# Kernel tuning notes

Measured on AMD Instinct MI355X. Metric: run time of the kernel, lower is better.

The kernel has to match this reference:

```python
import jax, jax.numpy as jnp
import numpy as np

N = 50000      # nodes
E = 800000     # edges (avg degree 16)
D = 64         # num_node_features
H = 64         # hidden_channels
G = 512        # graphs in batch
OUT = 32       # final linear output
NEG_SLOPE = 0.2


def setup_inputs() -> dict:
    key = jax.random.key(0)
    ks = jax.random.split(key, 20)
    s = 0.1  # param init scale
    inp = {
        "x": jax.random.normal(ks[0], (N, D), jnp.float32),
        "edge_index": jax.random.randint(ks[1], (2, E), 0, N, dtype=jnp.int64),
        "batch": jnp.sort(jax.random.randint(ks[2], (N,), 0, G, dtype=jnp.int64)),
        # GATv2 layer 1 (D -> H)
        "Wl1": jax.random.normal(ks[3], (D, H), jnp.float32) * s,
        "bl1": jnp.zeros((H,), jnp.float32),
        "Wr1": jax.random.normal(ks[4], (D, H), jnp.float32) * s,
        "br1": jnp.zeros((H,), jnp.float32),
        "att1": jax.random.normal(ks[5], (H,), jnp.float32) * s,
        "bias1": jnp.zeros((H,), jnp.float32),
        # GATv2 layer 2 (H -> H)
        "Wl2": jax.random.normal(ks[6], (H, H), jnp.float32) * s,
        "bl2": jnp.zeros((H,), jnp.float32),
        "Wr2": jax.random.normal(ks[7], (H, H), jnp.float32) * s,
        "br2": jnp.zeros((H,), jnp.float32),
        "att2": jax.random.normal(ks[8], (H,), jnp.float32) * s,
        "bias2": jnp.zeros((H,), jnp.float32),
        # final classifier
        "lin_w": jax.random.normal(ks[9], (H, OUT), jnp.float32) * s,
        "lin_b": jnp.zeros((OUT,), jnp.float32),
    }
    return inp


def _gatv2(x, src, dst, Wl, bl, Wr, br, att, bias):
    # GATv2Conv, heads=1, PyG semantics: messages flow src -> dst
    xl = x @ Wl + bl                       # [N, H] source transform (also the message)
    xr = x @ Wr + br                       # [N, H] destination transform
    z = xl[src] + xr[dst]                  # [E, H] gather
    e = jax.nn.leaky_relu(z, NEG_SLOPE) @ att  # [E] edge scores
    # segment softmax over edges grouped by destination node
    m = jax.ops.segment_max(e, dst, num_segments=N)   # [N]
    ex = jnp.exp(e - m[dst])                          # [E]
    denom = jax.ops.segment_sum(ex, dst, num_segments=N)  # [N]
    alpha = ex / denom[dst]                            # [E]
    out = jax.ops.segment_sum(alpha[:, None] * xl[src], dst, num_segments=N)  # [N, H]
    return out + bias


def reference(x, edge_index, batch,
              Wl1, bl1, Wr1, br1, att1, bias1,
              Wl2, bl2, Wr2, br2, att2, bias2,
              lin_w, lin_b):
    src, dst = edge_index[0], edge_index[1]
    h = jax.nn.relu(_gatv2(x, src, dst, Wl1, bl1, Wr1, br1, att1, bias1))
    h = jax.nn.relu(_gatv2(h, src, dst, Wl2, bl2, Wr2, br2, att2, bias2))
    # global mean pool over graphs
    sums = jax.ops.segment_sum(h, batch, num_segments=G)          # [G, H]
    cnts = jax.ops.segment_sum(jnp.ones((h.shape[0],), h.dtype), batch, num_segments=G)
    pooled = sums / jnp.maximum(cnts, 1.0)[:, None]
    # dropout(p=0.5) is identity at inference
    return pooled @ lin_w + lin_b                                  # [G, 32]
```

## Files before the change

kernel.cpp:

```cpp
#include <hip/hip_runtime.h>
#include <hip/hip_fp16.h>
#include <math.h>


#define ELLC    48
#define OVF_CAP 65536
#define ECHUNK  2048

typedef int      vint4 __attribute__((ext_vector_type(4)));
typedef _Float16 half4 __attribute__((ext_vector_type(4)));
typedef float    f32x4 __attribute__((ext_vector_type(4)));

#define GROWS 32

__device__ __forceinline__ void stage_rows_f32(
    int row0, int t, const float* __restrict__ X, int n, float* xS) {
    for (int i = t; i < GROWS * 16; i += 256) {
        int r = row0 + (i >> 4);
        f32x4 v;
        v[0] = 0.f; v[1] = 0.f; v[2] = 0.f; v[3] = 0.f;
        if (r < n)
            v = __builtin_nontemporal_load(
                &((const f32x4*)(X + (size_t)r * 64))[i & 15]);
        ((f32x4*)xS)[i] = v;
    }
}

__device__ __forceinline__ void gemm_compute(
    int row0, int t,
    const float* __restrict__ Wl, const float* __restrict__ bl,
    const float* __restrict__ Wr, const float* __restrict__ br,
    _Float16* __restrict__ xl, float* __restrict__ xr, int n,
    const float* xS) {
    int h  = t & 63;
    int rb = t >> 6;
    float accl[8], accr[8];
#pragma unroll
    for (int i = 0; i < 8; ++i) { accl[i] = 0.f; accr[i] = 0.f; }
#pragma unroll 4
    for (int d = 0; d < 64; ++d) {
        float wl = Wl[d * 64 + h];
        float wr = Wr[d * 64 + h];
#pragma unroll
        for (int i = 0; i < 8; ++i) {
            float xv = xS[(rb + 4 * i) * 64 + d];
            accl[i] += xv * wl;
            accr[i] += xv * wr;
        }
    }
    float blv = bl[h], brv = br[h];
#pragma unroll
    for (int i = 0; i < 8; ++i) {
        int r = row0 + rb + 4 * i;
        if (r < n) {
            __builtin_nontemporal_store((_Float16)(accl[i] + blv),
                                        &xl[(size_t)r * 64 + h]);
            __builtin_nontemporal_store(accr[i] + brv,
                                        &xr[(size_t)r * 64 + h]);
        }
    }
}

__global__ __launch_bounds__(256) void fill_gemm_kernel(
    const int* __restrict__ src, const int* __restrict__ dst,
    int* __restrict__ cnt, unsigned short* __restrict__ ell,
    int* __restrict__ novf, int* __restrict__ ovf_dst, int* __restrict__ ovf_src,
    int E, int N, int psize, int fb, int ggrid,
    const float* __restrict__ X,
    const float* __restrict__ Wl, const float* __restrict__ bl,
    const float* __restrict__ Wr, const float* __restrict__ br,
    _Float16* __restrict__ xl, float* __restrict__ xr) {
    __shared__ float xS[GROWS * 64];
    int b = blockIdx.x;
    int q = b / 24, r = b % 24;
    if (r >= 16) {
        int vg = q * 8 + (r - 16);
        if (vg < ggrid) {
            stage_rows_f32(vg * GROWS, threadIdx.x, X, N, xS);
            __syncthreads();
            gemm_compute(vg * GROWS, threadIdx.x, Wl, bl, Wr, br, xl, xr, N, xS);
        }
        return;
    }
    int vb = q * 16 + r;
    if (vb >= fb) return;
    int t     = threadIdx.x;
    int chunk = vb >> 3;
    int p     = vb & 7;
    int d0    = p * psize;
    int d1    = min(N, d0 + psize);
    int e0    = chunk * ECHUNK;
    int e1    = min(E, e0 + ECHUNK);
    int nq    = (e1 - e0) >> 2;
    const vint4* dst4 = (const vint4*)(dst + e0);
    const vint4* src4 = (const vint4*)(src + e0);

    auto scatter4 = [&](vint4 dv, vint4 sv) {
#pragma unroll
        for (int k = 0; k < 4; ++k) {
            int d = dv[k];
            int s = sv[k];
            if (d >= d0 && d < d1) {
                int pos = atomicAdd(&cnt[d], 1);
                if (pos < ELLC) {
                    ell[d * ELLC + pos] = (unsigned short)s;
                } else {
                    int j = atomicAdd(novf, 1);
                    if (j < OVF_CAP) { ovf_dst[j] = d; ovf_src[j] = s; }
                }
            }
        }
    };

    if (nq == (ECHUNK >> 2)) {
        vint4 dvA = __builtin_nontemporal_load(&dst4[t]);
        vint4 svA = __builtin_nontemporal_load(&src4[t]);
        vint4 dvB = __builtin_nontemporal_load(&dst4[t + 256]);
        vint4 svB = __builtin_nontemporal_load(&src4[t + 256]);
        scatter4(dvA, svA);
        scatter4(dvB, svB);
    } else {
        for (int qq = t; qq < nq; qq += 256) {
            vint4 dv = __builtin_nontemporal_load(&dst4[qq]);
            vint4 sv = __builtin_nontemporal_load(&src4[qq]);
            scatter4(dv, sv);
        }
        for (int e = e0 + (nq << 2) + t; e < e1; e += 256) {
            int d = dst[e];
            if (d >= d0 && d < d1) {
                int pos = atomicAdd(&cnt[d], 1);
                int s   = src[e];
                if (pos < ELLC) {
                    ell[d * ELLC + pos] = (unsigned short)s;
                } else {
                    int j = atomicAdd(novf, 1);
                    if (j < OVF_CAP) { ovf_dst[j] = d; ovf_src[j] = s; }
                }
            }
        }
    }
}

__device__ __forceinline__ void agg_row(
    int d, int lane, int g, int l,
    const _Float16* __restrict__ xl, const float* __restrict__ xr,
    const int* __restrict__ cnt, const unsigned short* __restrict__ ell,
    const int* __restrict__ novf, const int* __restrict__ ovf_dst,
    const int* __restrict__ ovf_src,
    float4 att4, float& s, float4& acc, int& deg_d) {
    deg_d = cnt[d];
    int nd  = min(deg_d, ELLC);
    int beg = d * ELLC;
    s = 0.f;
    acc = make_float4(0.f, 0.f, 0.f, 0.f);
    if (deg_d <= 0) return;

    int myidx = 0;
    if (lane < ELLC)
        myidx = (int)__builtin_nontemporal_load(&ell[beg + lane]);
    int i_first = __shfl(myidx, 0);

    f32x4 xrt = __builtin_nontemporal_load(
        &((const f32x4*)(xr + (size_t)d * 64))[l]);
    float4 xr4 = make_float4(xrt[0], xrt[1], xrt[2], xrt[3]);

#pragma unroll 6
    for (int k = 0; k * 8 < nd; ++k) {
        int  sa = k * 8 + g, sb = sa + 4;
        bool aa = sa < nd,   ab = sb < nd;
        int  i0 = __shfl(myidx, sa); if (!aa) i0 = i_first;
        int  i1 = __shfl(myidx, sb); if (!ab) i1 = i_first;
        half4 h0 = ((const half4*)(xl + (size_t)i0 * 64))[l];
        half4 h1 = ((const half4*)(xl + (size_t)i1 * 64))[l];
        float4 x0 = make_float4((float)h0[0], (float)h0[1], (float)h0[2], (float)h0[3]);
        float4 x1 = make_float4((float)h1[0], (float)h1[1], (float)h1[2], (float)h1[3]);
        float z, c0 = 0.f, c1 = 0.f;
        z = x0.x + xr4.x; c0 += ((z > 0.f) ? z : 0.2f * z) * att4.x;
        z = x0.y + xr4.y; c0 += ((z > 0.f) ? z : 0.2f * z) * att4.y;
        z = x0.z + xr4.z; c0 += ((z > 0.f) ? z : 0.2f * z) * att4.z;
        z = x0.w + xr4.w; c0 += ((z > 0.f) ? z : 0.2f * z) * att4.w;
        z = x1.x + xr4.x; c1 += ((z > 0.f) ? z : 0.2f * z) * att4.x;
        z = x1.y + xr4.y; c1 += ((z > 0.f) ? z : 0.2f * z) * att4.y;
        z = x1.z + xr4.z; c1 += ((z > 0.f) ? z : 0.2f * z) * att4.z;
        z = x1.w + xr4.w; c1 += ((z > 0.f) ? z : 0.2f * z) * att4.w;
#pragma unroll
        for (int sh = 8; sh >= 1; sh >>= 1) {
            c0 += __shfl_xor(c0, sh);
            c1 += __shfl_xor(c1, sh);
        }
        float w0 = aa ? __expf(fminf(c0, 30.f)) : 0.f;
        float w1 = ab ? __expf(fminf(c1, 30.f)) : 0.f;
        s += w0 + w1;
        acc.x += w0 * x0.x + w1 * x1.x;
        acc.y += w0 * x0.y + w1 * x1.y;
        acc.z += w0 * x0.z + w1 * x1.z;
        acc.w += w0 * x0.w + w1 * x1.w;
    }
    if (deg_d > ELLC) {
        int no = min(*novf, OVF_CAP);
        for (int j = g; j < no; j += 4) {
            bool active = (ovf_dst[j] == d);
            int  i0     = active ? ovf_src[j] : i_first;
            half4 h0 = ((const half4*)(xl + (size_t)i0 * 64))[l];
            float4 x0 = make_float4((float)h0[0], (float)h0[1], (float)h0[2], (float)h0[3]);
            f32x4 xrt2 = ((const f32x4*)(xr + (size_t)d * 64))[l];
            float z, c0 = 0.f;
            z = x0.x + xrt2[0]; c0 += ((z > 0.f) ? z : 0.2f * z) * att4.x;
            z = x0.y + xrt2[1]; c0 += ((z > 0.f) ? z : 0.2f * z) * att4.y;
            z = x0.z + xrt2[2]; c0 += ((z > 0.f) ? z : 0.2f * z) * att4.z;
            z = x0.w + xrt2[3]; c0 += ((z > 0.f) ? z : 0.2f * z) * att4.w;
#pragma unroll
            for (int sh = 8; sh >= 1; sh >>= 1) c0 += __shfl_xor(c0, sh);
            float w0 = active ? __expf(fminf(c0, 30.f)) : 0.f;
            s += w0;
            acc.x += w0 * x0.x;
            acc.y += w0 * x0.y;
            acc.z += w0 * x0.z;
            acc.w += w0 * x0.w;
        }
    }
#pragma unroll
    for (int mask = 16; mask <= 32; mask <<= 1) {
        s     += __shfl_xor(s, mask);
        acc.x += __shfl_xor(acc.x, mask);
        acc.y += __shfl_xor(acc.y, mask);
        acc.z += __shfl_xor(acc.z, mask);
        acc.w += __shfl_xor(acc.w, mask);
    }
}

__global__ __launch_bounds__(256) void agg_gemm_kernel(
    const _Float16* __restrict__ xl1, const float* __restrict__ xr1,
    const int* __restrict__ cnt, const unsigned short* __restrict__ ell,
    const int* __restrict__ novf, const int* __restrict__ ovf_dst,
    const int* __restrict__ ovf_src,
    const float* __restrict__ att, const float* __restrict__ bias,
    const float* __restrict__ Wl2, const float* __restrict__ bl2,
    const float* __restrict__ Wr2, const float* __restrict__ br2,
    _Float16* __restrict__ xl2, float* __restrict__ xr2, int n) {
    __shared__ float xS[GROWS * 64];
    int t    = threadIdx.x;
    int w    = t >> 6;
    int lane = t & 63;
    int g    = lane >> 4;
    int l    = lane & 15;
    int row0 = blockIdx.x * GROWS;

    float4 att4 = ((const float4*)att)[l];
    float4 b4   = ((const float4*)bias)[l];

    for (int i = 0; i < 8; ++i) {
        int rr = w * 8 + i;
        int d  = row0 + rr;
        float s; float4 acc; int deg_d;
        if (d < n) {
            agg_row(d, lane, g, l, xl1, xr1, cnt, ell, novf, ovf_dst, ovf_src,
                    att4, s, acc, deg_d);
        } else { s = 0.f; acc = make_float4(0.f, 0.f, 0.f, 0.f); }
        if (g == 0) {
            float4 hv = make_float4(0.f, 0.f, 0.f, 0.f);
            if (d < n) {
                float inv = (s > 0.f) ? (1.f / s) : 0.f;
                hv.x = fmaxf(acc.x * inv + b4.x, 0.f);
                hv.y = fmaxf(acc.y * inv + b4.y, 0.f);
                hv.z = fmaxf(acc.z * inv + b4.z, 0.f);
                hv.w = fmaxf(acc.w * inv + b4.w, 0.f);
            }
            ((float4*)(xS + rr * 64))[l] = hv;
        }
    }
    __syncthreads();
    gemm_compute(row0, t, Wl2, bl2, Wr2, br2, xl2, xr2, n, xS);
}

__global__ __launch_bounds__(256) void gat_aggregate_kernel(
    const _Float16* __restrict__ xl, const float* __restrict__ xr,
    const int* __restrict__ cnt, const unsigned short* __restrict__ ell,
    const int* __restrict__ novf, const int* __restrict__ ovf_dst,
    const int* __restrict__ ovf_src,
    const float* __restrict__ att, const float* __restrict__ bias,
    _Float16* __restrict__ out, int n) {
    int wid  = (blockIdx.x * blockDim.x + threadIdx.x) >> 6;
    int lane = threadIdx.x & 63;
    if (wid >= n) return;
    int g = lane >> 4;
    int l = lane & 15;
    float4 att4 = ((const float4*)att)[l];
    float4 b4   = ((const float4*)bias)[l];
    float s; float4 acc; int deg_d;
    agg_row(wid, lane, g, l, xl, xr, cnt, ell, novf, ovf_dst, ovf_src,
            att4, s, acc, deg_d);
    if (g == 0) {
        float inv = (s > 0.f) ? (1.f / s) : 0.f;
        half4 hv;
        hv[0] = (_Float16)fmaxf(acc.x * inv + b4.x, 0.f);
        hv[1] = (_Float16)fmaxf(acc.y * inv + b4.y, 0.f);
        hv[2] = (_Float16)fmaxf(acc.z * inv + b4.z, 0.f);
        hv[3] = (_Float16)fmaxf(acc.w * inv + b4.w, 0.f);
        __builtin_nontemporal_store(hv, (half4*)(out + (size_t)wid * 64) + l);
    }
}

__global__ __launch_bounds__(256) void pool_final_kernel(
    const _Float16* __restrict__ h, const int* __restrict__ batch,
    const float* __restrict__ lin_w, const float* __restrict__ lin_b,
    float* __restrict__ out, int N, int G) {
    int g = blockIdx.x;
    int t = threadIdx.x;
    auto lb = [&](int key) {
        int lo = 0, hi = N;
        while (lo < hi) {
            int mid = (lo + hi) >> 1;
            if (batch[mid] < key) lo = mid + 1; else hi = mid;
        }
        return lo;
    };
    int start = lb(g), end = lb(g + 1);

    __shared__ float part[4][64];
    __shared__ float pooled[64];
    int f = t & 63, w = t >> 6;
    float acc = 0.f;
    for (int i = start + w; i < end; i += 4)
        acc += (float)__builtin_nontemporal_load(&h[(size_t)i * 64 + f]);
    part[w][f] = acc;
    __syncthreads();
    if (t < 64) {
        float s = part[0][t] + part[1][t] + part[2][t] + part[3][t];
        pooled[t] = s / fmaxf((float)(end - start), 1.f);
    }
    __syncthreads();
    if (t < 32) {
        float a = 0.f;
#pragma unroll 8
        for (int hh = 0; hh < 64; ++hh) a += pooled[hh] * lin_w[hh * 32 + t];
        out[g * 32 + t] = a + lin_b[t];
    }
}

extern "C" void kernel_launch(void* const* d_in, const int* in_sizes, int n_in,
                              void* d_out, int out_size, void* d_ws, size_t ws_size,
                              hipStream_t stream) {
    const float* x     = (const float*)d_in[0];
    const int*   ei    = (const int*)d_in[1];
    const int*   batch = (const int*)d_in[2];
    const float* Wl1   = (const float*)d_in[3];
    const float* bl1   = (const float*)d_in[4];
    const float* Wr1   = (const float*)d_in[5];
    const float* br1   = (const float*)d_in[6];
    const float* att1  = (const float*)d_in[7];
    const float* bias1 = (const float*)d_in[8];
    const float* Wl2   = (const float*)d_in[9];
    const float* bl2   = (const float*)d_in[10];
    const float* Wr2   = (const float*)d_in[11];
    const float* br2   = (const float*)d_in[12];
    const float* att2  = (const float*)d_in[13];
    const float* bias2 = (const float*)d_in[14];
    const float* lin_w = (const float*)d_in[15];
    const float* lin_b = (const float*)d_in[16];
    float* out = (float*)d_out;

    const int N = in_sizes[0] / 64;
    const int E = in_sizes[1] / 2;
    const int G = out_size / 32;
    const int* src = ei;
    const int* dst = ei + E;

    char*  ws  = (char*)d_ws;
    size_t off = 0;
    auto alloc = [&](size_t bytes) -> void* {
        void* p = ws + off;
        off += bytes;
        off = (off + 255) & ~(size_t)255;
        return p;
    };
    _Float16* xl1  = (_Float16*)alloc((size_t)N * 64 * sizeof(_Float16));
    float* xr1     = (float*)alloc((size_t)N * 64 * sizeof(float));
    _Float16* xl2  = (_Float16*)alloc((size_t)N * 64 * sizeof(_Float16));
    float* xr2     = (float*)alloc((size_t)N * 64 * sizeof(float));
    _Float16* h2   = (_Float16*)alloc((size_t)N * 64 * sizeof(_Float16));
    int*   cnt     = (int*)alloc((size_t)N * sizeof(int));
    int*   novf    = (int*)alloc(256);
    char*  zend    = ws + off;
    unsigned short* ell = (unsigned short*)alloc((size_t)N * ELLC * sizeof(unsigned short));
    int*   ovf_dst = (int*)alloc((size_t)OVF_CAP * sizeof(int));
    int*   ovf_src = (int*)alloc((size_t)OVF_CAP * sizeof(int));

    (void)hipMemsetAsync(cnt, 0, (size_t)(zend - (char*)cnt), stream);

    int ggrid  = (N + GROWS - 1) / GROWS;
    int agrid  = (N + 3) / 4;
    int nchunk = (E + ECHUNK - 1) / ECHUNK;
    int fb     = nchunk * 8;
    int psize  = (N + 7) / 8;
    int ngroups = max((fb + 15) / 16, (ggrid + 7) / 8);
    int igrid   = ngroups * 24;

    fill_gemm_kernel<<<igrid, 256, 0, stream>>>(
        src, dst, cnt, ell, novf, ovf_dst, ovf_src, E, N, psize, fb, ggrid,
        x, Wl1, bl1, Wr1, br1, xl1, xr1);

    agg_gemm_kernel<<<ggrid, 256, 0, stream>>>(
        xl1, xr1, cnt, ell, novf, ovf_dst, ovf_src, att1, bias1,
        Wl2, bl2, Wr2, br2, xl2, xr2, N);

    gat_aggregate_kernel<<<agrid, 256, 0, stream>>>(
        xl2, xr2, cnt, ell, novf, ovf_dst, ovf_src, att2, bias2, h2, N);

    pool_final_kernel<<<G, 256, 0, stream>>>(h2, batch, lin_w, lin_b, out, N, G);
}
```

Baseline: 247.9 us.

## Fuse layer-2 aggregation with mean pooling and final linear per graph

The separate layer-2 aggregation kernel and pooling kernel become one kernel. There is one 1024-thread block per graph, and each wave aggregates the destination nodes of that graph. It accumulates ReLU outputs in registers and then reduces them through shared memory before the final linear. This removes writing and re-reading the fp16 h2 buffer and drops one kernel launch. The cost is a coarser grid of only G blocks, which may be imbalanced when graph sizes vary. The overflow path also reuses the already-loaded xr row instead of reloading it.

```diff
diff --git a/kernel.cpp b/kernel.cpp
--- a/kernel.cpp
+++ b/kernel.cpp
@@ -147,8 +147,8 @@
     const int* __restrict__ cnt, const unsigned short* __restrict__ ell,
     const int* __restrict__ novf, const int* __restrict__ ovf_dst,
     const int* __restrict__ ovf_src,
-    float4 att4, float& s, float4& acc, int& deg_d) {
-    deg_d = cnt[d];
+    float4 att4, float& s, float4& acc) {
+    int deg_d = cnt[d];
     int nd  = min(deg_d, ELLC);
     int beg = d * ELLC;
     s = 0.f;
@@ -203,12 +203,11 @@
             int  i0     = active ? ovf_src[j] : i_first;
             half4 h0 = ((const half4*)(xl + (size_t)i0 * 64))[l];
             float4 x0 = make_float4((float)h0[0], (float)h0[1], (float)h0[2], (float)h0[3]);
-            f32x4 xrt2 = ((const f32x4*)(xr + (size_t)d * 64))[l];
             float z, c0 = 0.f;
-            z = x0.x + xrt2[0]; c0 += ((z > 0.f) ? z : 0.2f * z) * att4.x;
-            z = x0.y + xrt2[1]; c0 += ((z > 0.f) ? z : 0.2f * z) * att4.y;
-            z = x0.z + xrt2[2]; c0 += ((z > 0.f) ? z : 0.2f * z) * att4.z;
-            z = x0.w + xrt2[3]; c0 += ((z > 0.f) ? z : 0.2f * z) * att4.w;
+            z = x0.x + xr4.x; c0 += ((z > 0.f) ? z : 0.2f * z) * att4.x;
+            z = x0.y + xr4.y; c0 += ((z > 0.f) ? z : 0.2f * z) * att4.y;
+            z = x0.z + xr4.z; c0 += ((z > 0.f) ? z : 0.2f * z) * att4.z;
+            z = x0.w + xr4.w; c0 += ((z > 0.f) ? z : 0.2f * z) * att4.w;
 #pragma unroll
             for (int sh = 8; sh >= 1; sh >>= 1) c0 += __shfl_xor(c0, sh);
             float w0 = active ? __expf(fminf(c0, 30.f)) : 0.f;
@@ -252,10 +251,10 @@
     for (int i = 0; i < 8; ++i) {
         int rr = w * 8 + i;
         int d  = row0 + rr;
-        float s; float4 acc; int deg_d;
+        float s; float4 acc;
         if (d < n) {
             agg_row(d, lane, g, l, xl1, xr1, cnt, ell, novf, ovf_dst, ovf_src,
-                    att4, s, acc, deg_d);
+                    att4, s, acc);
         } else { s = 0.f; acc = make_float4(0.f, 0.f, 0.f, 0.f); }
         if (g == 0) {
             float4 hv = make_float4(0.f, 0.f, 0.f, 0.f);
@@ -273,40 +272,22 @@
     gemm_compute(row0, t, Wl2, bl2, Wr2, br2, xl2, xr2, n, xS);
 }
 
-__global__ __launch_bounds__(256) void gat_aggregate_kernel(
+__global__ __launch_bounds__(1024) void agg_pool_final_kernel(
     const _Float16* __restrict__ xl, const float* __restrict__ xr,
     const int* __restrict__ cnt, const unsigned short* __restrict__ ell,
     const int* __restrict__ novf, const int* __restrict__ ovf_dst,
     const int* __restrict__ ovf_src,
     const float* __restrict__ att, const float* __restrict__ bias,
-    _Float16* __restrict__ out, int n) {
-    int wid  = (blockIdx.x * blockDim.x + threadIdx.x) >> 6;
-    int lane = threadIdx.x & 63;
-    if (wid >= n) return;
-    int g = lane >> 4;
-    int l = lane & 15;
-    float4 att4 = ((const float4*)att)[l];
-    float4 b4   = ((const float4*)bias)[l];
-    float s; float4 acc; int deg_d;
-    agg_row(wid, lane, g, l, xl, xr, cnt, ell, novf, ovf_dst, ovf_src,
-            att4, s, acc, deg_d);
-    if (g == 0) {
-        float inv = (s > 0.f) ? (1.f / s) : 0.f;
-        half4 hv;
-        hv[0] = (_Float16)fmaxf(acc.x * inv + b4.x, 0.f);
-        hv[1] = (_Float16)fmaxf(acc.y * inv + b4.y, 0.f);
-        hv[2] = (_Float16)fmaxf(acc.z * inv + b4.z, 0.f);
-        hv[3] = (_Float16)fmaxf(acc.w * inv + b4.w, 0.f);
-        __builtin_nontemporal_store(hv, (half4*)(out + (size_t)wid * 64) + l);
-    }
-}
-
-__global__ __launch_bounds__(256) void pool_final_kernel(
-    const _Float16* __restrict__ h, const int* __restrict__ batch,
+    const int* __restrict__ batch,
     const float* __restrict__ lin_w, const float* __restrict__ lin_b,
     float* __restrict__ out, int N, int G) {
-    int g = blockIdx.x;
-    int t = threadIdx.x;
+    int gid  = blockIdx.x;
+    int t    = threadIdx.x;
+    int w    = t >> 6;
+    int lane = t & 63;
+    int g    = lane >> 4;
+    int l    = lane & 15;
+
     auto lb = [&](int key) {
         int lo = 0, hi = N;
         while (lo < hi) {
@@ -315,26 +296,39 @@
         }
         return lo;
     };
-    int start = lb(g), end = lb(g + 1);
-
-    __shared__ float part[4][64];
+    int start = lb(gid), end = lb(gid + 1);
+
+    float4 att4 = ((const float4*)att)[l];
+    float4 b4   = ((const float4*)bias)[l];
+
+    float4 pool4 = make_float4(0.f, 0.f, 0.f, 0.f);
+    for (int d = start + w; d < end; d += 16) {
+        float s; float4 acc;
+        agg_row(d, lane, g, l, xl, xr, cnt, ell, novf, ovf_dst, ovf_src,
+                att4, s, acc);
+        float inv = (s > 0.f) ? (1.f / s) : 0.f;
+        pool4.x += fmaxf(acc.x * inv + b4.x, 0.f);
+        pool4.y += fmaxf(acc.y * inv + b4.y, 0.f);
+        pool4.z += fmaxf(acc.z * inv + b4.z, 0.f);
+        pool4.w += fmaxf(acc.w * inv + b4.w, 0.f);
+    }
+
+    __shared__ float part[16][64];
     __shared__ float pooled[64];
-    int f = t & 63, w = t >> 6;
-    float acc = 0.f;
-    for (int i = start + w; i < end; i += 4)
-        acc += (float)__builtin_nontemporal_load(&h[(size_t)i * 64 + f]);
-    part[w][f] = acc;
+    if (g == 0) ((float4*)part[w])[l] = pool4;
     __syncthreads();
     if (t < 64) {
-        float s = part[0][t] + part[1][t] + part[2][t] + part[3][t];
-        pooled[t] = s / fmaxf((float)(end - start), 1.f);
+        float sum = 0.f;
+#pragma unroll
+        for (int ww = 0; ww < 16; ++ww) sum += part[ww][t];
+        pooled[t] = sum / fmaxf((float)(end - start), 1.f);
     }
     __syncthreads();
     if (t < 32) {
         float a = 0.f;
 #pragma unroll 8
         for (int hh = 0; hh < 64; ++hh) a += pooled[hh] * lin_w[hh * 32 + t];
-        out[g * 32 + t] = a + lin_b[t];
+        out[gid * 32 + t] = a + lin_b[t];
     }
 }
 
@@ -378,7 +372,6 @@
     float* xr1     = (float*)alloc((size_t)N * 64 * sizeof(float));
     _Float16* xl2  = (_Float16*)alloc((size_t)N * 64 * sizeof(_Float16));
     float* xr2     = (float*)alloc((size_t)N * 64 * sizeof(float));
-    _Float16* h2   = (_Float16*)alloc((size_t)N * 64 * sizeof(_Float16));
     int*   cnt     = (int*)alloc((size_t)N * sizeof(int));
     int*   novf    = (int*)alloc(256);
     char*  zend    = ws + off;
@@ -389,7 +382,6 @@
     (void)hipMemsetAsync(cnt, 0, (size_t)(zend - (char*)cnt), stream);
 
     int ggrid  = (N + GROWS - 1) / GROWS;
-    int agrid  = (N + 3) / 4;
     int nchunk = (E + ECHUNK - 1) / ECHUNK;
     int fb     = nchunk * 8;
     int psize  = (N + 7) / 8;
@@ -404,8 +396,7 @@
         xl1, xr1, cnt, ell, novf, ovf_dst, ovf_src, att1, bias1,
         Wl2, bl2, Wr2, br2, xl2, xr2, N);
 
-    gat_aggregate_kernel<<<agrid, 256, 0, stream>>>(
-        xl2, xr2, cnt, ell, novf, ovf_dst, ovf_src, att2, bias2, h2, N);
-
-    pool_final_kernel<<<G, 256, 0, stream>>>(h2, batch, lin_w, lin_b, out, N, G);
-}
+    agg_pool_final_kernel<<<G, 1024, 0, stream>>>(
+        xl2, xr2, cnt, ell, novf, ovf_dst, ovf_src, att2, bias2,
+        batch, lin_w, lin_b, out, N, G);
+}
```

Result: slower. 254.5 us (+2.7%).
